# Optimization experiments

Measured on AMD Instinct MI355X. Metric: run time of the kernel, lower is better.

The kernel has to match this reference:

```python
import jax, jax.numpy as jnp
import numpy as np

DIM = 384
INNER = DIM * 4            # expansion_factor=4 -> inner_dim=1536
E = 5                      # num_experts
K = 2                      # num_actives
KS = 31                    # conv kernel size
SQ = DIM // 8              # senet squeeze dim
B, T = 4, 1024


def _p(key, shape, scale=0.02):
    return jax.random.normal(key, shape, dtype=jnp.float32) * scale


def setup_inputs() -> dict:
    key = jax.random.key(0)
    ks = jax.random.split(key, 24)
    return {
        "res": jax.random.normal(ks[0], (B, T, DIM), dtype=jnp.float32),
        # LayerNorm
        "ln_g": jnp.ones((DIM,), jnp.float32),
        "ln_b": jnp.zeros((DIM,), jnp.float32),
        # depthwise Conv1d (groups=dim): kernel [dim, 1, ks]
        "conv_w": _p(ks[1], (DIM, 1, KS)),
        "conv_b": _p(ks[2], (DIM,)),
        # router: Linear(dim,dim) -> SiLU -> Linear(dim,E)
        "rw1": _p(ks[3], (DIM, DIM)), "rb1": jnp.zeros((DIM,), jnp.float32),
        "rw2": _p(ks[4], (DIM, E)),  "rb2": jnp.zeros((E,), jnp.float32),
        # stacked expert weights
        "we1": _p(ks[5], (E, DIM, 2 * INNER)),   "be1": jnp.zeros((E, 2 * INNER), jnp.float32),
        "we2": _p(ks[6], (E, INNER, 2 * INNER)), "be2": jnp.zeros((E, 2 * INNER), jnp.float32),
        "we3": _p(ks[7], (E, INNER, DIM)),       "be3": jnp.zeros((E, DIM), jnp.float32),
        # senet
        "sw1": _p(ks[8], (DIM, SQ)), "sb1": jnp.zeros((SQ,), jnp.float32),
        "sw2": _p(ks[9], (SQ, DIM)), "sb2": jnp.zeros((DIM,), jnp.float32),
        "senet_res": jnp.ones((DIM,), jnp.float32),
    }


def _layernorm(x, g, b, eps=1e-5):
    mu = jnp.mean(x, axis=-1, keepdims=True)
    var = jnp.mean(jnp.square(x - mu), axis=-1, keepdims=True)
    return (x - mu) * jax.lax.rsqrt(var + eps) * g + b


def _swiglu(h):
    a, g = jnp.split(h, 2, axis=-1)
    return a * jax.nn.silu(g)


def _forward(res, ln_g, ln_b, conv_w, conv_b, rw1, rb1, rw2, rb2,
             we1, be1, we2, be2, we3, be3, sw1, sb1, sw2, sb2, senet_res):
    x = _layernorm(res, ln_g, ln_b)                       # [B,T,D]
    # depthwise conv over time (eval mode, no dropout)
    xt = jnp.transpose(x, (0, 2, 1))                      # [B,D,T]
    c = jax.lax.conv_general_dilated(
        xt, conv_w, window_strides=(1,), padding=[(KS // 2, KS // 2)],
        feature_group_count=DIM, dimension_numbers=("NCH", "OIH", "NCH"))
    h = jnp.transpose(c + conv_b[None, :, None], (0, 2, 1))  # [B,T,D]

    # ---- MoE (eval: no routing noise). Dense-equivalent combine: tokens not
    # routed to an expert get softmax weight exactly 0, so weighted sum matches
    # the original gather/scatter_add math. ----
    tok = h.reshape(B * T, DIM)                           # [N,D]
    rv = jax.nn.silu(tok @ rw1 + rb1) @ rw2 + rb2         # [N,E]
    _, top_idx = jax.lax.top_k(rv, K)                     # [N,K]
    n = tok.shape[0]
    mask = jnp.zeros((n, E), bool).at[jnp.arange(n)[:, None], top_idx].set(True)
    w = jax.nn.softmax(jnp.where(mask, rv, -jnp.inf), axis=1)  # [N,E]

    h1 = _swiglu(jnp.einsum("nd,edh->enh", tok, we1) + be1[:, None, :])  # [E,N,INNER]
    h2 = _swiglu(jnp.einsum("enh,ehk->enk", h1, we2) + be2[:, None, :])  # [E,N,INNER]
    eo = jnp.einsum("enh,ehd->end", h2, we3) + be3[:, None, :]           # [E,N,D]
    y = (tok + jnp.einsum("ne,end->nd", w, eo)).reshape(B, T, DIM)

    # senet gate
    pooled = jnp.mean(x * senet_res + y, axis=-2)          # [B,D]
    gate = jax.nn.sigmoid(jax.nn.silu(pooled @ sw1 + sb1) @ sw2 + sb2)
    return res + y * gate[:, None, :]


def reference(res, ln_g, ln_b, conv_w, conv_b, rw1, rb1, rw2, rb2,
              we1, be1, we2, be2, we3, be3, sw1, sb1, sw2, sb2, senet_res):
    return _forward(res, ln_g, ln_b, conv_w, conv_b, rw1, rb1, rw2, rb2,
                    we1, be1, we2, be2, we3, be3, sw1, sb1, sw2, sb2, senet_res)
```

## Files before the change

kernel.cpp:

```cpp
#include <hip/hip_runtime.h>
#include <stdint.h>

#define DIM 384
#define INNER 1536
#define H2X 3072
#define NE 5
#define NB 4
#define NT 1024
#define NN (NB*NT)
#define KSZ 31
#define SQZ 48
#define NASSIGN (NN*2)

typedef float floatx4 __attribute__((ext_vector_type(4)));
typedef __bf16 bf16x8 __attribute__((ext_vector_type(8)));

__device__ __forceinline__ unsigned short f2bs(float f){
  union { float f; uint32_t u; } v; v.f = f;
  uint32_t r = (v.u + 0x7fffu + ((v.u >> 16) & 1u)) >> 16;
  return (unsigned short)r;
}
__device__ __forceinline__ float bs2f(unsigned short s){
  union { uint32_t u; float f; } v; v.u = ((uint32_t)s) << 16; return v.f;
}
__device__ __forceinline__ float fsigmoid(float x){ return 1.f/(1.f+__expf(-x)); }

__device__ __forceinline__ uint32_t pk2_lo(float a, float b, uint32_t old){
  return __builtin_amdgcn_cvt_pk_fp8_f32(a, b, old, false);
}
__device__ __forceinline__ uint32_t pk2_hi(float a, float b, uint32_t old){
  return __builtin_amdgcn_cvt_pk_fp8_f32(a, b, old, true);
}
__device__ __forceinline__ uint8_t f2fp8(float a){
  return (uint8_t)__builtin_amdgcn_cvt_pk_fp8_f32(a, 0.f, 0u, false);
}

__device__ __forceinline__ void gload16(const void* g, void* l){
  __builtin_amdgcn_global_load_lds(
    reinterpret_cast<const __attribute__((address_space(1))) unsigned int*>(
        reinterpret_cast<uintptr_t>(g)),
    reinterpret_cast<__attribute__((address_space(3))) unsigned int*>(
        (unsigned int)reinterpret_cast<uintptr_t>(l)),
    16, 0, 0);
}

__device__ __forceinline__ int prefix_cnt(const int* __restrict__ cnt, int e){
  int base = 0;
  #pragma unroll
  for(int k=0;k<NE;k++) base += (k<e) ? cnt[k] : 0;
  return base;
}

#define WSCALE 8.f

__device__ __forceinline__ void do_tr_bf16(const float* __restrict__ in,
    unsigned short* __restrict__ out, int R, int C, int cx, int cy){
  __shared__ float tile[32][65];
  int c0 = cx*32, r0 = cy*64;
  int tx = threadIdx.x, ty = threadIdx.y;
  #pragma unroll
  for (int i=0;i<8;i++){
    int r = ty + i*8;
    tile[tx][r] = in[(size_t)(r0+r)*C + c0 + tx];
  }
  __syncthreads();
  #pragma unroll
  for (int i=0;i<4;i++){
    int c = ty + i*8;
    uint32_t lo = f2bs(tile[c][2*tx]);
    uint32_t hi = f2bs(tile[c][2*tx+1]);
    *(uint32_t*)&out[(size_t)(c0+c)*R + r0 + 2*tx] = lo | (hi<<16);
  }
}
__device__ __forceinline__ void do_tr_fp8(const float* __restrict__ in,
    uint8_t* __restrict__ out, int R, int C, int cx, int cy){
  __shared__ float tile[32][65];
  int c0 = cx*32, r0 = cy*64;
  int tx = threadIdx.x, ty = threadIdx.y;
  #pragma unroll
  for (int i=0;i<8;i++){
    int r = ty + i*8;
    tile[tx][r] = in[(size_t)(r0+r)*C + c0 + tx];
  }
  __syncthreads();
  #pragma unroll
  for (int i=0;i<4;i++){
    int c = ty + i*8;
    uint32_t v = pk2_lo(tile[c][2*tx]*WSCALE, tile[c][2*tx+1]*WSCALE, 0u);
    *(unsigned short*)&out[(size_t)(c0+c)*R + r0 + 2*tx] = (unsigned short)(v & 0xffffu);
  }
}

#define TR_N1 (96*6*5)
#define TR_N2 (96*24*5)
#define TR_N3 (12*24*5)
#define TR_N4 (12*6)
__global__ __launch_bounds__(256) void tr_all_kernel(
    const float* __restrict__ we1, uint8_t* __restrict__ w1t,
    const float* __restrict__ we2, uint8_t* __restrict__ w2t,
    const float* __restrict__ we3, uint8_t* __restrict__ w3t,
    const float* __restrict__ rw1, unsigned short* __restrict__ rw1t){
  int bid = blockIdx.x;
  if (bid < TR_N1){
    int z = bid/(96*6), rem = bid%(96*6);
    do_tr_fp8(we1 + (size_t)z*384*3072, w1t + (size_t)z*384*3072, 384, 3072, rem%96, rem/96);
  } else if (bid < TR_N1+TR_N2){
    int idx = bid - TR_N1;
    int z = idx/(96*24), rem = idx%(96*24);
    do_tr_fp8(we2 + (size_t)z*1536*3072, w2t + (size_t)z*1536*3072, 1536, 3072, rem%96, rem/96);
  } else if (bid < TR_N1+TR_N2+TR_N3){
    int idx = bid - TR_N1 - TR_N2;
    int z = idx/(12*24), rem = idx%(12*24);
    do_tr_fp8(we3 + (size_t)z*1536*384, w3t + (size_t)z*1536*384, 1536, 384, rem%12, rem/12);
  } else {
    int idx = bid - TR_N1 - TR_N2 - TR_N3;
    do_tr_bf16(rw1, rw1t, 384, 384, idx%12, idx/12);
  }
}

#define CTT 16
__global__ __launch_bounds__(384) void convln_kernel(const float* __restrict__ res,
    const float* __restrict__ ln_g, const float* __restrict__ ln_b,
    const float* __restrict__ cw, const float* __restrict__ cb,
    float* __restrict__ x, unsigned short* __restrict__ tokb, float* __restrict__ y){
  __shared__ float tile[(CTT+30)*DIM];
  int b = blockIdx.y, t0 = blockIdx.x*CTT;
  int tid = threadIdx.x;
  int w = tid>>6, lane = tid&63;
  float gw[6], bw[6];
  #pragma unroll
  for(int i=0;i<6;i++){ gw[i]=ln_g[i*64+lane]; bw[i]=ln_b[i*64+lane]; }
  for(int r=w; r<CTT+30; r+=6){
    int gt = t0 - 15 + r;
    if(gt>=0 && gt<NT){
      const float* rp = res + ((size_t)b*NT+gt)*DIM;
      float v[6]; float s=0.f;
      #pragma unroll
      for(int i=0;i<6;i++){ v[i]=rp[i*64+lane]; s+=v[i]; }
      #pragma unroll
      for(int o=32;o;o>>=1) s += __shfl_down(s,o);
      s = __shfl(s,0);
      float mean = s*(1.f/DIM);
      float q=0.f;
      #pragma unroll
      for(int i=0;i<6;i++){ v[i]-=mean; q+=v[i]*v[i]; }
      #pragma unroll
      for(int o=32;o;o>>=1) q += __shfl_down(q,o);
      q = __shfl(q,0);
      float rstd = rsqrtf(q*(1.f/DIM) + 1e-5f);
      #pragma unroll
      for(int i=0;i<6;i++) tile[r*DIM+i*64+lane] = v[i]*rstd*gw[i]+bw[i];
    } else {
      #pragma unroll
      for(int i=0;i<6;i++) tile[r*DIM+i*64+lane] = 0.f;
    }
  }
  __syncthreads();
  float cwr[KSZ];
  #pragma unroll
  for(int k=0;k<KSZ;k++) cwr[k] = cw[tid*KSZ+k];
  float bias = cb[tid];
  float win[CTT+30];
  #pragma unroll
  for(int r=0;r<CTT+30;r++) win[r] = tile[r*DIM+tid];
  #pragma unroll
  for(int t=0;t<CTT;t++){
    float acc = bias;
    #pragma unroll
    for(int k=0;k<KSZ;k++) acc += win[t+k]*cwr[k];
    size_t o = ((size_t)b*NT + t0 + t)*DIM + tid;
    y[o]=acc; tokb[o]=f2bs(acc);
    x[o]=win[t+15];
  }
}

__global__ __launch_bounds__(256) void router_g1_kernel(const unsigned short* __restrict__ tokb,
    const unsigned short* __restrict__ rw1t, const float* __restrict__ rb1,
    unsigned short* __restrict__ g1, int* __restrict__ cnt){
  int tid = threadIdx.x;
  if(blockIdx.x==0 && blockIdx.y==0 && tid<32) cnt[tid]=0;
  __shared__ alignas(16) unsigned short sA0[128*32];
  __shared__ alignas(16) unsigned short sA1[128*32];
  __shared__ alignas(16) unsigned short sB0[128*32];
  __shared__ alignas(16) unsigned short sB1[128*32];
  int n0 = blockIdx.x*128, m0 = blockIdx.y*128;
  int lane = tid&63, wid = tid>>6, wm = wid&1, wn = wid>>1;
  int l15 = lane&15, quad = lane>>4;
  floatx4 acc[4][4];
  #pragma unroll
  for(int i=0;i<4;i++)
    #pragma unroll
    for(int j=0;j<4;j++) acc[i][j]=(floatx4){0.f,0.f,0.f,0.f};
  int rA = tid>>2, c8 = tid&3;
  const unsigned short* a0p = tokb + (size_t)(m0+rA)*DIM;
  const unsigned short* a1p = tokb + (size_t)(m0+64+rA)*DIM;
  const unsigned short* b0p = rw1t + (size_t)(n0+rA)*DIM;
  const unsigned short* b1p = rw1t + (size_t)(n0+64+rA)*DIM;

  auto stage = [&](int kt, unsigned short* dA, unsigned short* dB){
    gload16(a0p + kt + c8*8, dA + wid*512);
    gload16(a1p + kt + c8*8, dA + 2048 + wid*512);
    gload16(b0p + kt + c8*8, dB + wid*512);
    gload16(b1p + kt + c8*8, dB + 2048 + wid*512);
  };
  auto compute = [&](const unsigned short* cA, const unsigned short* cB){
    bf16x8 af[4], bfr[4];
    #pragma unroll
    for(int mi=0;mi<4;mi++) af[mi] = *(const bf16x8*)&cA[(wm*64+mi*16+l15)*32 + quad*8];
    #pragma unroll
    for(int ni=0;ni<4;ni++) bfr[ni] = *(const bf16x8*)&cB[(wn*64+ni*16+l15)*32 + quad*8];
    #pragma unroll
    for(int mi=0;mi<4;mi++)
      #pragma unroll
      for(int ni=0;ni<4;ni++)
        acc[mi][ni] = __builtin_amdgcn_mfma_f32_16x16x32_bf16(af[mi], bfr[ni], acc[mi][ni],0,0,0);
  };

  stage(0, sA0, sB0);
  __syncthreads();
  for(int kt=0; kt<DIM; kt+=64){
    if (kt+32 < DIM) stage(kt+32, sA1, sB1);
    compute(sA0, sB0);
    __syncthreads();
    if (kt+64 < DIM) stage(kt+64, sA0, sB0);
    compute(sA1, sB1);
    __syncthreads();
  }
  #pragma unroll
  for(int ni=0;ni<4;ni++){
    int col = n0 + wn*64 + ni*16 + l15;
    float bias = rb1[col];
    #pragma unroll
    for(int mi=0;mi<4;mi++){
      int rowb = m0 + wm*64 + mi*16 + quad*4;
      #pragma unroll
      for(int r=0;r<4;r++){
        float v = acc[mi][ni][r] + bias;
        g1[(size_t)(rowb+r)*DIM + col] = f2bs(v*fsigmoid(v));
      }
    }
  }
}

__global__ __launch_bounds__(256) void router2_kernel(const unsigned short* __restrict__ g1,
    const float* __restrict__ rw2, const float* __restrict__ rb2,
    int* __restrict__ ridx, float* __restrict__ rwt, int* __restrict__ cnt){
  __shared__ int hist[8];
  int tid = threadIdx.x;
  int wid = tid>>6, lane = tid&63;
  if(tid<8) hist[tid]=0;
  __syncthreads();
  for(int it=0; it<8; ++it){
    int n = blockIdx.x*32 + wid*8 + it;
    float s[NE]={0.f,0.f,0.f,0.f,0.f};
    #pragma unroll
    for(int i=0;i<6;i++){
      int d = lane + i*64;
      float gv = bs2f(g1[(size_t)n*DIM+d]);
      #pragma unroll
      for(int e=0;e<NE;e++) s[e] += gv * rw2[d*NE+e];
    }
    #pragma unroll
    for(int e=0;e<NE;e++)
      #pragma unroll
      for(int o=32;o;o>>=1) s[e] += __shfl_down(s[e],o);
    if(lane==0){
      float r[NE];
      #pragma unroll
      for(int e=0;e<NE;e++) r[e]=s[e]+rb2[e];
      int e0=0;
      for(int e=1;e<NE;e++) if(r[e]>r[e0]) e0=e;
      int e1=-1;
      for(int e=0;e<NE;e++){ if(e==e0) continue; if(e1<0||r[e]>r[e1]) e1=e; }
      float w0 = 1.f/(1.f+__expf(r[e1]-r[e0]));
      ridx[2*n]=e0; ridx[2*n+1]=e1;
      rwt[2*n]=w0; rwt[2*n+1]=1.f-w0;
      atomicAdd(&hist[e0],1); atomicAdd(&hist[e1],1);
    }
  }
  __syncthreads();
  if(tid<NE) atomicAdd(&cnt[tid], hist[tid]);
}

__global__ __launch_bounds__(256) void fillcompact_kernel(const int* __restrict__ ridx,
    const int* __restrict__ cnt, int* __restrict__ cnt2,
    int* __restrict__ inv, const unsigned short* __restrict__ tokb,
    uint8_t* __restrict__ tokc, float* __restrict__ pooled){
  __shared__ int sSrc[32], sPos[32];
  int tid = threadIdx.x;
  if(blockIdx.x==0){
    for(int i=tid;i<NB*DIM;i+=256) pooled[i]=0.f;
  }
  int lane = tid&63;
  if(tid<64){
    int i = blockIdx.x*32 + lane;
    int e = (lane<32) ? ridx[i] : -1;
    int base = (lane<32) ? prefix_cnt(cnt, e) : 0;
    unsigned long long below = (1ull<<lane)-1ull;
    int pos = 0;
    #pragma unroll
    for(int ex=0; ex<NE; ex++){
      unsigned long long m = __ballot(e==ex);
      if(m){
        int ldr = __ffsll((long long)m)-1;
        int nb = 0;
        if(lane==ldr) nb = atomicAdd(&cnt2[ex], (int)__popcll(m));
        nb = __shfl(nb, ldr);
        if(e==ex) pos = base + nb + (int)__popcll(m & below);
      }
    }
    if(lane<32){
      inv[i] = pos;
      sSrc[lane] = i>>1;
      sPos[lane] = pos;
    }
  }
  __syncthreads();
  int w = tid>>6;
  for(int j=0;j<8;j++){
    int idx = w*8+j;
    int src = sSrc[idx], dst = sPos[idx];
    if(lane<48){
      uint4 sv = ((const uint4*)&tokb[(size_t)src*DIM])[lane];
      float f0=bs2f(sv.x&0xffff)*WSCALE, f1=bs2f(sv.x>>16)*WSCALE;
      float f2=bs2f(sv.y&0xffff)*WSCALE, f3=bs2f(sv.y>>16)*WSCALE;
      float f4=bs2f(sv.z&0xffff)*WSCALE, f5=bs2f(sv.z>>16)*WSCALE;
      float f6=bs2f(sv.w&0xffff)*WSCALE, f7=bs2f(sv.w>>16)*WSCALE;
      uint32_t lo = pk2_hi(f2,f3, pk2_lo(f0,f1,0u));
      uint32_t hi = pk2_hi(f6,f7, pk2_lo(f4,f5,0u));
      uint2 pv; pv.x = lo; pv.y = hi;
      ((uint2*)&tokc[(size_t)dst*DIM])[lane] = pv;
    }
  }
}

template<int KDIM>
__device__ __forceinline__ void gemm_swiglu_impl(
    const uint8_t* __restrict__ A,
    const uint8_t* __restrict__ wt, const float* __restrict__ bias,
    const int* __restrict__ cnt, uint8_t* __restrict__ out,
    float inv_scale, float out_scale, int xtile, int mtile, int e){
  int cn = cnt[e];
  if (mtile*64 >= cn) return;
  int base = prefix_cnt(cnt, e);
  int j0 = xtile*128;
  int tid=threadIdx.x, lane=tid&63, wid=tid>>6;
  int l15=lane&15, quad=lane>>4;
  __shared__ alignas(16) uint8_t sA0[64*64];
  __shared__ alignas(16) uint8_t sA1[64*64];
  __shared__ alignas(16) uint8_t sBa0[128*64];
  __shared__ alignas(16) uint8_t sBa1[128*64];
  __shared__ alignas(16) uint8_t sBg0[128*64];
  __shared__ alignas(16) uint8_t sBg1[128*64];
  int rA = tid>>2;
  int gb = ((tid&3) ^ ((tid>>3)&3))*16;
  const uint8_t* a0p = A + (size_t)(base + min(mtile*64+rA, cn-1))*KDIM + gb;
  const uint8_t* b0p = wt + ((size_t)e*H2X + j0 + rA)*KDIM + gb;
  const uint8_t* b1p = wt + ((size_t)e*H2X + j0 + 64 + rA)*KDIM + gb;
  const uint8_t* g0p = wt + ((size_t)e*H2X + INNER + j0 + rA)*KDIM + gb;
  const uint8_t* g1p = wt + ((size_t)e*H2X + INNER + j0 + 64 + rA)*KDIM + gb;
  floatx4 aca[4][2], acg[4][2];
  #pragma unroll
  for(int i=0;i<4;i++)
    #pragma unroll
    for(int j=0;j<2;j++){ aca[i][j]=(floatx4){0.f,0.f,0.f,0.f}; acg[i][j]=(floatx4){0.f,0.f,0.f,0.f}; }
  int ldsw = wid*1024;

  auto stage = [&](int kt, uint8_t* dA, uint8_t* dBa, uint8_t* dBg){
    gload16(a0p + kt, dA + ldsw);
    gload16(b0p + kt, dBa + ldsw);
    gload16(b1p + kt, dBa + 4096 + ldsw);
    gload16(g0p + kt, dBg + ldsw);
    gload16(g1p + kt, dBg + 4096 + ldsw);
  };
  auto compute = [&](const uint8_t* cA, const uint8_t* cBa, const uint8_t* cBg){
    #pragma unroll
    for(int s=0;s<2;s++){
      int pq = (((s*4+quad) ^ (l15&6)))*8;
      long af[4], ba[2], bg[2];
      #pragma unroll
      for(int mi=0;mi<4;mi++) af[mi] = *(const long*)&cA[(mi*16+l15)*64 + pq];
      #pragma unroll
      for(int ni=0;ni<2;ni++){
        int col = wid*32 + ni*16 + l15;
        ba[ni] = *(const long*)&cBa[col*64 + pq];
        bg[ni] = *(const long*)&cBg[col*64 + pq];
      }
      #pragma unroll
      for(int mi=0;mi<4;mi++)
        #pragma unroll
        for(int ni=0;ni<2;ni++){
          aca[mi][ni] = __builtin_amdgcn_mfma_f32_16x16x32_fp8_fp8(af[mi], ba[ni], aca[mi][ni],0,0,0);
          acg[mi][ni] = __builtin_amdgcn_mfma_f32_16x16x32_fp8_fp8(af[mi], bg[ni], acg[mi][ni],0,0,0);
        }
    }
  };

  stage(0, sA0, sBa0, sBg0);
  __syncthreads();
  for(int kt=0; kt<KDIM; kt+=128){
    if (kt+64 < KDIM) stage(kt+64, sA1, sBa1, sBg1);
    compute(sA0, sBa0, sBg0);
    __syncthreads();
    if (kt+128 < KDIM) stage(kt+128, sA0, sBa0, sBg0);
    compute(sA1, sBa1, sBg1);
    __syncthreads();
  }

  #pragma unroll
  for(int ni=0;ni<2;ni++){
    int j = j0 + wid*32 + ni*16 + l15;
    float ba_ = bias[e*H2X + j];
    float bg_ = bias[e*H2X + INNER + j];
    #pragma unroll
    for(int mi=0;mi<4;mi++){
      int rl = mi*16 + quad*4;
      #pragma unroll
      for(int r=0;r<4;r++){
        int row = mtile*64 + rl + r;
        if(row < cn){
          float a = aca[mi][ni][r]*inv_scale + ba_;
          float g = acg[mi][ni][r]*inv_scale + bg_;
          out[(size_t)(base+row)*INNER + j] = f2fp8(a*g*fsigmoid(g)*out_scale);
        }
      }
    }
  }
}

#define SG_NX (INNER/128)
#define SG_NY (NN/64)
__global__ __launch_bounds__(256,3) void gemm_sg1_kernel(
    const uint8_t* __restrict__ A, const uint8_t* __restrict__ wt,
    const float* __restrict__ bias, const int* __restrict__ cnt, uint8_t* __restrict__ out){
  int id = blockIdx.x;
  int y = id % SG_NY, xe = id / SG_NY;
  gemm_swiglu_impl<DIM>(A, wt, bias, cnt, out, 1.f/64.f, 64.f, xe % SG_NX, y, xe / SG_NX);
}
__global__ __launch_bounds__(256,3) void gemm_sg2_kernel(
    const uint8_t* __restrict__ A, const uint8_t* __restrict__ wt,
    const float* __restrict__ bias, const int* __restrict__ cnt, uint8_t* __restrict__ out){
  int id = blockIdx.x;
  int y = id % SG_NY, xe = id / SG_NY;
  gemm_swiglu_impl<INNER>(A, wt, bias, cnt, out, 1.f/512.f, 2097152.f, xe % SG_NX, y, xe / SG_NX);
}

__global__ __launch_bounds__(256,4) void gemm_out_kernel(
    const uint8_t* __restrict__ h2, const uint8_t* __restrict__ w3t,
    const float* __restrict__ be3, const int* __restrict__ cnt, float* __restrict__ eo){
  int e = blockIdx.z;
  int cn = cnt[e];
  int mtile = blockIdx.y;
  if (mtile*64 >= cn) return;
  int base = prefix_cnt(cnt, e);
  int jt = blockIdx.x % 3, kh = blockIdx.x / 3;
  int n0 = jt*128;
  int koff = kh*768;
  float* eos = eo + (size_t)kh*NASSIGN*DIM;
  int tid=threadIdx.x, lane=tid&63, wid=tid>>6;
  int l15=lane&15, quad=lane>>4;
  __shared__ alignas(16) uint8_t sA0[64*64];
  __shared__ alignas(16) uint8_t sA1[64*64];
  __shared__ alignas(16) uint8_t sB0[128*64];
  __shared__ alignas(16) uint8_t sB1[128*64];
  int rA = tid>>2;
  int gb = ((tid&3) ^ ((tid>>3)&3))*16;
  const uint8_t* a0p = h2 + (size_t)(base + min(mtile*64+rA, cn-1))*INNER + koff + gb;
  const uint8_t* b0p = w3t + ((size_t)e*DIM + n0 + rA)*INNER + koff + gb;
  const uint8_t* b1p = w3t + ((size_t)e*DIM + n0 + 64 + rA)*INNER + koff + gb;
  floatx4 acc[4][2];
  #pragma unroll
  for(int i=0;i<4;i++)
    #pragma unroll
    for(int j=0;j<2;j++) acc[i][j]=(floatx4){0.f,0.f,0.f,0.f};
  int ldsw = wid*1024;

  auto stage = [&](int kt, uint8_t* dA, uint8_t* dB){
    gload16(a0p + kt, dA + ldsw);
    gload16(b0p + kt, dB + ldsw);
    gload16(b1p + kt, dB + 4096 + ldsw);
  };
  auto compute = [&](const uint8_t* cA, const uint8_t* cB){
    #pragma unroll
    for(int s=0;s<2;s++){
      int pq = (((s*4+quad) ^ (l15&6)))*8;
      long af[4], bfr[2];
      #pragma unroll
      for(int mi=0;mi<4;mi++) af[mi] = *(const long*)&cA[(mi*16+l15)*64 + pq];
      #pragma unroll
      for(int ni=0;ni<2;ni++){
        int col = wid*32 + ni*16 + l15;
        bfr[ni] = *(const long*)&cB[col*64 + pq];
      }
      #pragma unroll
      for(int mi=0;mi<4;mi++)
        #pragma unroll
        for(int ni=0;ni<2;ni++)
          acc[mi][ni] = __builtin_amdgcn_mfma_f32_16x16x32_fp8_fp8(af[mi], bfr[ni], acc[mi][ni],0,0,0);
    }
  };

  stage(0, sA0, sB0);
  __syncthreads();
  for(int kt=0; kt<768; kt+=128){
    if (kt+64 < 768) stage(kt+64, sA1, sB1);
    compute(sA0, sB0);
    __syncthreads();
    if (kt+128 < 768) stage(kt+128, sA0, sB0);
    compute(sA1, sB1);
    __syncthreads();
  }

  const float OSC = 5.9604644775390625e-8f;
  #pragma unroll
  for(int ni=0;ni<2;ni++){
    int col = n0 + wid*32 + ni*16 + l15;
    float b3 = (kh==0) ? be3[e*DIM + col] : 0.f;
    #pragma unroll
    for(int mi=0;mi<4;mi++){
      int rl = mi*16 + quad*4;
      #pragma unroll
      for(int r=0;r<4;r++){
        int row = mtile*64 + rl + r;
        if(row < cn){
          eos[(size_t)(base+row)*DIM + col] = acc[mi][ni][r]*OSC + b3;
        }
      }
    }
  }
}

__global__ __launch_bounds__(384) void combine_pooled_kernel(const float* __restrict__ eo,
    const int* __restrict__ inv, const float* __restrict__ rwt,
    const float* __restrict__ x, const float* __restrict__ sres,
    float* __restrict__ y, float* __restrict__ pooled){
  int b = blockIdx.y, t0 = blockIdx.x*8;
  int d = threadIdx.x;
  const float* eo1 = eo + (size_t)NASSIGN*DIM;
  float sr = sres[d];
  float acc = 0.f;
  for(int t=0;t<8;t++){
    int n = b*NT + t0 + t;
    int p0 = inv[2*n], p1 = inv[2*n+1];
    float w0 = rwt[2*n], w1 = rwt[2*n+1];
    size_t o = (size_t)n*DIM + d;
    float yv = y[o] + w0*(eo[(size_t)p0*DIM+d] + eo1[(size_t)p0*DIM+d])
                    + w1*(eo[(size_t)p1*DIM+d] + eo1[(size_t)p1*DIM+d]);
    y[o] = yv;
    acc += x[o]*sr + yv;
  }
  atomicAdd(&pooled[b*DIM+d], acc*(1.f/NT));
}

__global__ __launch_bounds__(384) void gatefinal_kernel(const float* __restrict__ pooled,
    const float* __restrict__ sw1, const float* __restrict__ sb1,
    const float* __restrict__ sw2, const float* __restrict__ sb2,
    const float* __restrict__ res, const float* __restrict__ y, float* __restrict__ out){
  int b = blockIdx.y, t0 = blockIdx.x*8;
  int d = threadIdx.x;
  __shared__ float sp[DIM];
  __shared__ float sh[SQZ];
  sp[d] = pooled[b*DIM+d];
  __syncthreads();
  if(d<SQZ){
    float a = sb1[d];
    for(int k=0;k<DIM;k++) a += sp[k]*sw1[k*SQZ+d];
    sh[d] = a*fsigmoid(a);
  }
  __syncthreads();
  float a = sb2[d];
  #pragma unroll
  for(int j=0;j<SQZ;j++) a += sh[j]*sw2[j*DIM+d];
  float g = fsigmoid(a);
  for(int t=0;t<8;t++){
    size_t o = ((size_t)b*NT + t0 + t)*DIM + d;
    out[o] = res[o] + y[o]*g;
  }
}

extern "C" void kernel_launch(void* const* d_in, const int* in_sizes, int n_in,
                              void* d_out, int out_size, void* d_ws, size_t ws_size,
                              hipStream_t stream) {
  (void)in_sizes; (void)n_in; (void)out_size; (void)ws_size;
  const float* res   = (const float*)d_in[0];
  const float* ln_g  = (const float*)d_in[1];
  const float* ln_b  = (const float*)d_in[2];
  const float* conv_w= (const float*)d_in[3];
  const float* conv_b= (const float*)d_in[4];
  const float* rw1   = (const float*)d_in[5];
  const float* rb1   = (const float*)d_in[6];
  const float* rw2   = (const float*)d_in[7];
  const float* rb2   = (const float*)d_in[8];
  const float* we1   = (const float*)d_in[9];
  const float* be1   = (const float*)d_in[10];
  const float* we2   = (const float*)d_in[11];
  const float* be2   = (const float*)d_in[12];
  const float* we3   = (const float*)d_in[13];
  const float* be3   = (const float*)d_in[14];
  const float* sw1   = (const float*)d_in[15];
  const float* sb1   = (const float*)d_in[16];
  const float* sw2   = (const float*)d_in[17];
  const float* sb2   = (const float*)d_in[18];
  const float* sres  = (const float*)d_in[19];
  float* out = (float*)d_out;

  char* ws = (char*)d_ws;
  size_t off = 0;
  auto alloc = [&](size_t bytes)->void*{ void* p = ws + off; off = (off + bytes + 255) & ~(size_t)255; return p; };
  float*          x     = (float*)alloc((size_t)NN*DIM*4);
  float*          y     = (float*)alloc((size_t)NN*DIM*4);
  float*          eo    = (float*)alloc((size_t)2*NASSIGN*DIM*4);
  unsigned short* tokb  = (unsigned short*)alloc((size_t)NN*DIM*2);
  uint8_t*        tokc  = (uint8_t*)alloc((size_t)NASSIGN*DIM);
  unsigned short* g1    = (unsigned short*)alloc((size_t)NN*DIM*2);
  uint8_t*        w1t   = (uint8_t*)alloc((size_t)NE*H2X*DIM);
  uint8_t*        w2t   = (uint8_t*)alloc((size_t)NE*H2X*INNER);
  uint8_t*        w3t   = (uint8_t*)alloc((size_t)NE*DIM*INNER);
  unsigned short* rw1t  = (unsigned short*)alloc((size_t)DIM*DIM*2);
  uint8_t*        h1    = (uint8_t*)alloc((size_t)NASSIGN*INNER);
  uint8_t*        h2b   = (uint8_t*)alloc((size_t)NASSIGN*INNER);
  int*            ridx  = (int*)alloc((size_t)NASSIGN*4);
  float*          rwt   = (float*)alloc((size_t)NASSIGN*4);
  int*            inv   = (int*)alloc((size_t)NASSIGN*4);
  int*            cnt   = (int*)alloc(128);
  int*            cnt2  = cnt + 8;
  float*          pooled= (float*)alloc((size_t)NB*DIM*4);

  tr_all_kernel<<<TR_N1+TR_N2+TR_N3+TR_N4, dim3(32,8), 0, stream>>>(
      we1, w1t, we2, w2t, we3, w3t, rw1, rw1t);
  convln_kernel<<<dim3(NT/CTT, NB), 384, 0, stream>>>(
      res, ln_g, ln_b, conv_w, conv_b, x, tokb, y);
  router_g1_kernel<<<dim3(DIM/128, NN/128), 256, 0, stream>>>(tokb, rw1t, rb1, g1, cnt);
  router2_kernel<<<NN/32, 256, 0, stream>>>(g1, rw2, rb2, ridx, rwt, cnt);
  fillcompact_kernel<<<NASSIGN/32, 256, 0, stream>>>(ridx, cnt, cnt2, inv, tokb, tokc, pooled);

  gemm_sg1_kernel<<<SG_NX*SG_NY*NE, 256, 0, stream>>>(tokc, w1t, be1, cnt, h1);
  gemm_sg2_kernel<<<SG_NX*SG_NY*NE, 256, 0, stream>>>(h1, w2t, be2, cnt, h2b);
  gemm_out_kernel<<<dim3(6, NN/64, NE), 256, 0, stream>>>(h2b, w3t, be3, cnt, eo);
  combine_pooled_kernel<<<dim3(NT/8, NB), 384, 0, stream>>>(
      eo, inv, rwt, x, sres, y, pooled);
  gatefinal_kernel<<<dim3(NT/8, NB), 384, 0, stream>>>(
      pooled, sw1, sb1, sw2, sb2, res, y, out);
}
```

Before: 455.2 us.

## Use fine-grained vmcnt waits and 3D grid in SwiGLU expert GEMMs

Replaces __syncthreads in the double-buffered SwiGLU GEMM loop with raw s_barrier plus explicit s_waitcnt vmcnt(5), so the prefetch of the next K tile stays in flight while the current tile is computed. It also changes the launch from a flat 1D grid, where M tiles varied fastest, to a 3D grid with the N tile in x. That changes block scheduling order and so which blocks share weights in L2. The hand-written vmcnt count depends on how many loads stage issues, and it is fragile if the compiler reorders or splits those loads.

```diff
diff --git a/kernel.cpp b/kernel.cpp
--- a/kernel.cpp
+++ b/kernel.cpp
@@ -339,11 +339,13 @@
     const uint8_t* __restrict__ A,
     const uint8_t* __restrict__ wt, const float* __restrict__ bias,
     const int* __restrict__ cnt, uint8_t* __restrict__ out,
-    float inv_scale, float out_scale, int xtile, int mtile, int e){
+    float inv_scale, float out_scale){
+  int e = blockIdx.z;
   int cn = cnt[e];
+  int mtile = blockIdx.y;
   if (mtile*64 >= cn) return;
   int base = prefix_cnt(cnt, e);
-  int j0 = xtile*128;
+  int j0 = blockIdx.x*128;
   int tid=threadIdx.x, lane=tid&63, wid=tid>>6;
   int l15=lane&15, quad=lane>>4;
   __shared__ alignas(16) uint8_t sA0[64*64];
@@ -396,15 +398,24 @@
     }
   };
 
+  constexpr int nt = KDIM/64;
   stage(0, sA0, sBa0, sBg0);
-  __syncthreads();
-  for(int kt=0; kt<KDIM; kt+=128){
-    if (kt+64 < KDIM) stage(kt+64, sA1, sBa1, sBg1);
+  #pragma unroll 1
+  for(int t=0; t<nt; t+=2){
+    stage((t+1)*64, sA1, sBa1, sBg1);
+    asm volatile("s_waitcnt vmcnt(5)" ::: "memory");
+    __builtin_amdgcn_s_barrier();
     compute(sA0, sBa0, sBg0);
-    __syncthreads();
-    if (kt+128 < KDIM) stage(kt+128, sA0, sBa0, sBg0);
+    __builtin_amdgcn_s_barrier();
+    if (t+2 < nt){
+      stage((t+2)*64, sA0, sBa0, sBg0);
+      asm volatile("s_waitcnt vmcnt(5)" ::: "memory");
+    } else {
+      asm volatile("s_waitcnt vmcnt(0)" ::: "memory");
+    }
+    __builtin_amdgcn_s_barrier();
     compute(sA1, sBa1, sBg1);
-    __syncthreads();
+    __builtin_amdgcn_s_barrier();
   }
 
   #pragma unroll
@@ -428,21 +439,15 @@
   }
 }
 
-#define SG_NX (INNER/128)
-#define SG_NY (NN/64)
 __global__ __launch_bounds__(256,3) void gemm_sg1_kernel(
     const uint8_t* __restrict__ A, const uint8_t* __restrict__ wt,
     const float* __restrict__ bias, const int* __restrict__ cnt, uint8_t* __restrict__ out){
-  int id = blockIdx.x;
-  int y = id % SG_NY, xe = id / SG_NY;
-  gemm_swiglu_impl<DIM>(A, wt, bias, cnt, out, 1.f/64.f, 64.f, xe % SG_NX, y, xe / SG_NX);
+  gemm_swiglu_impl<DIM>(A, wt, bias, cnt, out, 1.f/64.f, 64.f);
 }
 __global__ __launch_bounds__(256,3) void gemm_sg2_kernel(
     const uint8_t* __restrict__ A, const uint8_t* __restrict__ wt,
     const float* __restrict__ bias, const int* __restrict__ cnt, uint8_t* __restrict__ out){
-  int id = blockIdx.x;
-  int y = id % SG_NY, xe = id / SG_NY;
-  gemm_swiglu_impl<INNER>(A, wt, bias, cnt, out, 1.f/512.f, 2097152.f, xe % SG_NX, y, xe / SG_NX);
+  gemm_swiglu_impl<INNER>(A, wt, bias, cnt, out, 1.f/512.f, 2097152.f);
 }
 
 __global__ __launch_bounds__(256,4) void gemm_out_kernel(
@@ -634,8 +639,8 @@
   router2_kernel<<<NN/32, 256, 0, stream>>>(g1, rw2, rb2, ridx, rwt, cnt);
   fillcompact_kernel<<<NASSIGN/32, 256, 0, stream>>>(ridx, cnt, cnt2, inv, tokb, tokc, pooled);
 
-  gemm_sg1_kernel<<<SG_NX*SG_NY*NE, 256, 0, stream>>>(tokc, w1t, be1, cnt, h1);
-  gemm_sg2_kernel<<<SG_NX*SG_NY*NE, 256, 0, stream>>>(h1, w2t, be2, cnt, h2b);
+  gemm_sg1_kernel<<<dim3(INNER/128, NN/64, NE), 256, 0, stream>>>(tokc, w1t, be1, cnt, h1);
+  gemm_sg2_kernel<<<dim3(INNER/128, NN/64, NE), 256, 0, stream>>>(h1, w2t, be2, cnt, h2b);
   gemm_out_kernel<<<dim3(6, NN/64, NE), 256, 0, stream>>>(h2b, w3t, be3, cnt, eo);
   combine_pooled_kernel<<<dim3(NT/8, NB), 384, 0, stream>>>(
       eo, inv, rwt, x, sres, y, pooled);
```

Result: faster. 430.3 us (-5.5%).
